# Kernel optimization log

Measured on AMD Instinct MI355X. Metric: run time of the kernel, lower is better.

Reference implementation:

```python
import jax, jax.numpy as jnp
import numpy as np

T_ITERS, N_SLOTS, INPUT_DIM, DIM = 6, 256, 1024, 1024
MLP_DIM = DIM // 2
B, C, H, W = 8, 1024, 64, 64
LN_EPS = 1e-5


def _ln(x, g, b):
    m = jnp.mean(x, axis=-1, keepdims=True)
    v = jnp.mean(jnp.square(x - m), axis=-1, keepdims=True)
    return (x - m) * jax.lax.rsqrt(v + LN_EPS) * g + b


def setup_inputs() -> dict:
    key = jax.random.key(0)
    ks = jax.random.split(key, 8)
    x = jax.random.normal(ks[0], (B, C, H, W), dtype=jnp.float32)
    templates_init = jax.random.normal(ks[1], (1, N_SLOTS, DIM), dtype=jnp.float32)
    # torch Linear weight is [out,in]; store as [in,out] for x @ W
    s_in = 1.0 / np.sqrt(INPUT_DIM)
    s_d = 1.0 / np.sqrt(DIM)
    Wq = jax.random.uniform(ks[2], (DIM, DIM), jnp.float32, -s_d, s_d)
    Wk = jax.random.uniform(ks[3], (INPUT_DIM, DIM), jnp.float32, -s_in, s_in)
    Wv = jax.random.uniform(ks[4], (INPUT_DIM, DIM), jnp.float32, -s_in, s_in)
    W1 = jax.random.uniform(ks[5], (DIM, MLP_DIM), jnp.float32, -s_d, s_d)
    b1 = jnp.zeros((MLP_DIM,), jnp.float32)
    s_m = 1.0 / np.sqrt(MLP_DIM)
    W2 = jax.random.uniform(ks[6], (MLP_DIM, DIM), jnp.float32, -s_m, s_m)
    b2 = jnp.zeros((DIM,), jnp.float32)
    return {
        "x": x, "templates_init": templates_init,
        "Wq": Wq, "Wk": Wk, "Wv": Wv,
        "ln_in_g": jnp.ones((INPUT_DIM,), jnp.float32), "ln_in_b": jnp.zeros((INPUT_DIM,), jnp.float32),
        "ln_t_g": jnp.ones((DIM,), jnp.float32), "ln_t_b": jnp.zeros((DIM,), jnp.float32),
        "ln_m_g": jnp.ones((DIM,), jnp.float32), "ln_m_b": jnp.zeros((DIM,), jnp.float32),
        "W1": W1, "b1": b1, "W2": W2, "b2": b2,
    }


def reference(x, templates_init, Wq, Wk, Wv, ln_in_g, ln_in_b, ln_t_g, ln_t_b,
              ln_m_g, ln_m_b, W1, b1, W2, b2):
    Bv, Cv, Hv, Wd = x.shape
    scale = DIM ** (-0.5)
    xr = x.reshape(Bv, Cv, Hv * Wd).transpose(0, 2, 1)  # [B, L, C]
    xn = _ln(xr, ln_in_g, ln_in_b)
    k = xn @ Wk  # [B, L, D]
    v = xn @ Wv  # [B, L, D]
    templates = jnp.broadcast_to(templates_init, (Bv, N_SLOTS, DIM))
    attn = None
    for _ in range(T_ITERS):
        t_prev = templates
        t = _ln(t_prev, ln_t_g, ln_t_b)
        q = (t @ Wq) * scale  # [B, N, D]
        logits = jnp.einsum('bnd,bld->bln', q, k)
        attn = jax.nn.softmax(logits, axis=-1) + 1e-8  # softmax over N
        attn = attn / jnp.sum(attn, axis=-2, keepdims=True)  # renorm over L
        templates = t_prev + jnp.einsum('bld,bln->bnd', v, attn)
        m = _ln(templates, ln_m_g, ln_m_b)
        templates = templates + jax.nn.relu(m @ W1 + b1) @ W2 + b2
    out_templates = templates.transpose(0, 2, 1)[:, :, :, None]  # [B, D, N, 1]
    out_attn = attn.transpose(0, 2, 1).reshape(Bv, N_SLOTS, Hv, Wd)
    return (out_templates, out_attn)
```

## Files before the change

kernel.cpp:

```cpp
#include <hip/hip_runtime.h>

#define EPS_ 1e-5f
#define SCALE_ 0.03125f

typedef __attribute__((ext_vector_type(8))) short short8;
typedef __attribute__((ext_vector_type(4))) float f32x4;
typedef unsigned short u16;

__device__ __forceinline__ float bf2f(u16 s) {
  return __uint_as_float(((unsigned int)s) << 16);
}
__device__ __forceinline__ u16 f2bf(float f) {
  unsigned int u = __float_as_uint(f);
  unsigned int r = 0x7FFFu + ((u >> 16) & 1u);
  return (u16)((u + r) >> 16);
}

__device__ __forceinline__ void gload16(const void* g, void* l) {
  __builtin_amdgcn_global_load_lds(
      (const __attribute__((address_space(1))) unsigned int*)g,
      (__attribute__((address_space(3))) unsigned int*)l, 16, 0, 0);
}

__global__ __launch_bounds__(256) void ln_part(const float* __restrict__ x,
                                               float* __restrict__ ps,
                                               float* __restrict__ ps2) {
  int tl = threadIdx.x & 63;
  int cg = threadIdx.x >> 6;
  int lblk = blockIdx.x >> 3;
  int cchunk = blockIdx.x & 7;
  int row = lblk * 64 + tl;
  int bb = row >> 12, l = row & 4095;
  const float* xp = x + (long)bb * 4194304L + l;
  int c0 = cchunk * 128 + cg;
  float s = 0.f, s2 = 0.f;
#pragma unroll
  for (int i = 0; i < 32; ++i) {
    float v = xp[(long)(c0 + i * 4) * 4096];
    s += v; s2 += v * v;
  }
  __shared__ float sh[2][4][64];
  sh[0][cg][tl] = s; sh[1][cg][tl] = s2;
  __syncthreads();
  if (threadIdx.x < 64) {
    float ts = sh[0][0][tl] + sh[0][1][tl] + sh[0][2][tl] + sh[0][3][tl];
    float t2 = sh[1][0][tl] + sh[1][1][tl] + sh[1][2][tl] + sh[1][3][tl];
    ps[cchunk * 32768 + row] = ts;
    ps2[cchunk * 32768 + row] = t2;
  }
}

__global__ __launch_bounds__(256) void ln_red(const float* __restrict__ ps,
                                              const float* __restrict__ ps2,
                                              float* __restrict__ meanp,
                                              float* __restrict__ rstdp) {
  int row = blockIdx.x * 256 + threadIdx.x;
  float s = 0.f, s2 = 0.f;
#pragma unroll
  for (int k = 0; k < 8; ++k) {
    s += ps[k * 32768 + row];
    s2 += ps2[k * 32768 + row];
  }
  float mu = s * (1.0f / 1024.0f);
  float var = s2 * (1.0f / 1024.0f) - mu * mu;
  meanp[row] = mu;
  rstdp[row] = rsqrtf(var + EPS_);
}

__global__ __launch_bounds__(256) void xn_make(const float* __restrict__ x,
                                               u16* __restrict__ xn,
                                               const float* __restrict__ meanp,
                                               const float* __restrict__ rstdp,
                                               const float* __restrict__ g,
                                               const float* __restrict__ beta) {
  __shared__ float tile[32][33];
  int b = blockIdx.z;
  int ct = blockIdx.y * 32;
  int lt = blockIdx.x * 32;
  int tx = threadIdx.x & 31, ty = threadIdx.x >> 5;
  const float* xp = x + (long)b * 4194304;
  int l = lt + tx;
  float mu = meanp[(b << 12) + l];
  float rs = rstdp[(b << 12) + l];
#pragma unroll
  for (int k = 0; k < 32; k += 8) {
    int c = ct + ty + k;
    float v = xp[(long)c * 4096 + l];
    tile[ty + k][tx] = (v - mu) * rs * g[c] + beta[c];
  }
  __syncthreads();
  u16* xq = xn + (long)b * 4194304;
#pragma unroll
  for (int k = 0; k < 32; k += 8) {
    int ll = lt + ty + k;
    xq[(long)ll * 1024 + ct + tx] = f2bf(tile[tx][ty + k]);
  }
}

__global__ __launch_bounds__(256) void transpose_f32(const float* __restrict__ src,
                                                     float* __restrict__ dst,
                                                     int R, int Cc, long sSrc, long sDst) {
  __shared__ float tile[32][33];
  int z = blockIdx.z;
  int rt = blockIdx.y * 32, ct = blockIdx.x * 32;
  int tx = threadIdx.x & 31, ty = threadIdx.x >> 5;
  const float* s = src + (long)z * sSrc;
  float* d = dst + (long)z * sDst;
#pragma unroll
  for (int k = 0; k < 32; k += 8) tile[ty + k][tx] = s[(long)(rt + ty + k) * Cc + ct + tx];
  __syncthreads();
#pragma unroll
  for (int k = 0; k < 32; k += 8) d[(long)(ct + ty + k) * R + rt + tx] = tile[tx][ty + k];
}

__global__ __launch_bounds__(256) void tcast(const float* __restrict__ src,
                                             u16* __restrict__ dst, int R, int C) {
  __shared__ float tile[32][33];
  int rt = blockIdx.y * 32, ct = blockIdx.x * 32;
  int tx = threadIdx.x & 31, ty = threadIdx.x >> 5;
#pragma unroll
  for (int k = 0; k < 32; k += 8) tile[ty + k][tx] = src[(long)(rt + ty + k) * C + ct + tx];
  __syncthreads();
#pragma unroll
  for (int k = 0; k < 32; k += 8) dst[(long)(ct + ty + k) * R + rt + tx] = f2bf(tile[tx][ty + k]);
}

__global__ __launch_bounds__(256) void castbf(const float* __restrict__ in,
                                              u16* __restrict__ out) {
  long i = (long)blockIdx.x * 256 + threadIdx.x;
  out[i] = f2bf(in[i]);
}

enum { E_BF16 = 0, E_SCALEBF = 1, E_F32 = 2, E_UPD = 3, E_RELU = 4, E_ADDB = 5 };

template <int EPI, int KSPLIT = 1>
__global__ __launch_bounds__(256) void mgemm(
    const u16* __restrict__ A, const u16* __restrict__ Bt, void* __restrict__ Cv,
    int K, int lda, int ldb, int ldc, long sA, long sB, long sC,
    const float* __restrict__ bias, const float* __restrict__ colsum) {
  __shared__ u16 Als[128 * 64];
  __shared__ u16 Bls[128 * 64];
  const int tid = threadIdx.x;
  const int zb = (KSPLIT == 1) ? blockIdx.z : blockIdx.z / KSPLIT;
  const int ks = (KSPLIT == 1) ? 0 : blockIdx.z % KSPLIT;
  const int bm = blockIdx.y * 128;
  const int bn = blockIdx.x * 128;
  A += (long)zb * sA;
  Bt += (long)zb * sB;
  const int kpart = K / KSPLIT;
  const int kbase = ks * kpart;
  const int lane = tid & 63;
  const int w = tid >> 6;
  const int wm = (w & 1) * 64, wn = (w >> 1) * 64;
  const int fr = lane & 15;
  const int fq = lane >> 4;
  f32x4 acc[4][4] = {};

  const int srow = tid >> 3;
  const int sko = (tid & 7) << 3;
  const u16* Ag = A + (long)(bm + srow) * lda + kbase + sko;
  const u16* Bg = Bt + (long)(bn + srow) * ldb + kbase + sko;
  u16* Al = Als + tid * 8;
  u16* Bl = Bls + tid * 8;
  const long astep = 32L * lda;
  const long bstep = 32L * ldb;

  for (int k0 = 0; k0 < kpart; k0 += 64) {
#pragma unroll
    for (int i = 0; i < 4; ++i) {
      gload16(Ag + i * astep + k0, Al + i * 2048);
      gload16(Bg + i * bstep + k0, Bl + i * 2048);
    }
    __syncthreads();
#pragma unroll
    for (int kc = 0; kc < 2; ++kc) {
      const int koff = kc * 32 + fq * 8;
      short8 af[4], bf[4];
#pragma unroll
      for (int i = 0; i < 4; ++i)
        af[i] = *(const short8*)&Als[(wm + i * 16 + fr) * 64 + koff];
#pragma unroll
      for (int j = 0; j < 4; ++j)
        bf[j] = *(const short8*)&Bls[(wn + j * 16 + fr) * 64 + koff];
#pragma unroll
      for (int i = 0; i < 4; ++i)
#pragma unroll
        for (int j = 0; j < 4; ++j)
          acc[i][j] = __builtin_amdgcn_mfma_f32_16x16x32_bf16(af[i], bf[j], acc[i][j], 0, 0, 0);
    }
    __syncthreads();
  }

#pragma unroll
  for (int i = 0; i < 4; ++i) {
#pragma unroll
    for (int j = 0; j < 4; ++j) {
      int gc = bn + wn + j * 16 + fr;
#pragma unroll
      for (int r = 0; r < 4; ++r) {
        int gr = bm + wm + i * 16 + fq * 4 + r;
        float v = acc[i][j][r];
        if constexpr (EPI == E_BF16) {
          ((u16*)Cv + (long)zb * sC)[(long)gr * ldc + gc] = f2bf(v);
        } else if constexpr (EPI == E_SCALEBF) {
          ((u16*)Cv + (long)zb * sC)[(long)gr * ldc + gc] = f2bf(v * SCALE_);
        } else if constexpr (EPI == E_F32) {
          ((float*)Cv + (long)zb * sC)[(long)gr * ldc + gc] = v;
        } else if constexpr (EPI == E_UPD) {
          float* C = (float*)Cv + (long)zb * sC;
          float add = v * (1.0f / colsum[zb * 256 + gr]);
          if constexpr (KSPLIT > 1) atomicAdd(&C[(long)gr * ldc + gc], add);
          else C[(long)gr * ldc + gc] += add;
        } else if constexpr (EPI == E_RELU) {
          float h = v + bias[gc];
          ((u16*)Cv + (long)zb * sC)[(long)gr * ldc + gc] = f2bf(h > 0.f ? h : 0.f);
        } else {
          float* C = (float*)Cv + (long)zb * sC;
          C[(long)gr * ldc + gc] += v + bias[gc];
        }
      }
    }
  }
}

__global__ __launch_bounds__(256) void row_ln_bf(const float* __restrict__ in,
                                                 u16* __restrict__ out,
                                                 const float* __restrict__ g,
                                                 const float* __restrict__ bvec) {
  long base = (long)blockIdx.x * 1024;
  int c = threadIdx.x << 2;
  float4 xv = *(const float4*)&in[base + c];
  float s = xv.x + xv.y + xv.z + xv.w;
  float s2 = xv.x * xv.x + xv.y * xv.y + xv.z * xv.z + xv.w * xv.w;
#pragma unroll
  for (int off = 32; off > 0; off >>= 1) {
    s += __shfl_down(s, off);
    s2 += __shfl_down(s2, off);
  }
  __shared__ float sh[8];
  if ((threadIdx.x & 63) == 0) {
    sh[threadIdx.x >> 6] = s;
    sh[4 + (threadIdx.x >> 6)] = s2;
  }
  __syncthreads();
  float ts = sh[0] + sh[1] + sh[2] + sh[3];
  float t2 = sh[4] + sh[5] + sh[6] + sh[7];
  float mu = ts * (1.0f / 1024.0f);
  float rs = rsqrtf(t2 * (1.0f / 1024.0f) - mu * mu + EPS_);
  ushort4 o;
  o.x = f2bf((xv.x - mu) * rs * g[c + 0] + bvec[c + 0]);
  o.y = f2bf((xv.y - mu) * rs * g[c + 1] + bvec[c + 1]);
  o.z = f2bf((xv.z - mu) * rs * g[c + 2] + bvec[c + 2]);
  o.w = f2bf((xv.w - mu) * rs * g[c + 3] + bvec[c + 3]);
  *(ushort4*)&out[base + c] = o;
}

__global__ __launch_bounds__(256) void softmax_tile(const float* __restrict__ lg,
                                                    u16* __restrict__ attnbf) {
  __shared__ float tile[256 * 36];
  __shared__ float pmax[8][32], psum[8][32];
  __shared__ float fm[32], fi[32];
  const int z = blockIdx.y;
  const int lt = blockIdx.x * 32;
  const int t = threadIdx.x;
  const float* base = lg + (long)z * 1048576 + lt;
  const int lr = t >> 3, lcg = (t & 7) << 2;
#pragma unroll
  for (int p = 0; p < 8; ++p) {
    int n = p * 32 + lr;
    float4 v = *(const float4*)&base[(long)n * 4096 + lcg];
    *(float4*)&tile[n * 36 + lcg] = v;
  }
  __syncthreads();
  const int l = t & 31, g = t >> 5;
  float m = -1e30f;
#pragma unroll
  for (int i = 0; i < 32; ++i) m = fmaxf(m, tile[(g * 32 + i) * 36 + l]);
  pmax[g][l] = m;
  __syncthreads();
  if (t < 32) {
    float mm = pmax[0][t];
#pragma unroll
    for (int k = 1; k < 8; ++k) mm = fmaxf(mm, pmax[k][t]);
    fm[t] = mm;
  }
  __syncthreads();
  float mx = fm[l];
  float s = 0.f;
#pragma unroll
  for (int i = 0; i < 32; ++i) {
    int n = g * 32 + i;
    float e = __expf(tile[n * 36 + l] - mx);
    tile[n * 36 + l] = e;
    s += e;
  }
  psum[g][l] = s;
  __syncthreads();
  if (t < 32) {
    float ss = psum[0][t];
#pragma unroll
    for (int k = 1; k < 8; ++k) ss += psum[k][t];
    fi[t] = 1.0f / ss;
  }
  __syncthreads();
  float inv = fi[l];
  u16* outp = attnbf + (long)z * 1048576 + lt + l;
#pragma unroll
  for (int i = 0; i < 32; ++i) {
    int n = g * 32 + i;
    outp[(long)n * 4096] = f2bf(tile[n * 36 + l] * inv + 1e-8f);
  }
}

__global__ __launch_bounds__(256) void row_sum_bf(const u16* __restrict__ a,
                                                  float* __restrict__ colsum) {
  long base = (long)blockIdx.x * 4096 + threadIdx.x * 16;
  float s = 0.f;
#pragma unroll
  for (int i = 0; i < 16; i += 4) {
    ushort4 v = *(const ushort4*)&a[base + i];
    s += bf2f(v.x) + bf2f(v.y) + bf2f(v.z) + bf2f(v.w);
  }
#pragma unroll
  for (int off = 32; off > 0; off >>= 1) s += __shfl_down(s, off);
  __shared__ float sh[4];
  if ((threadIdx.x & 63) == 0) sh[threadIdx.x >> 6] = s;
  __syncthreads();
  if (threadIdx.x == 0) colsum[blockIdx.x] = sh[0] + sh[1] + sh[2] + sh[3];
}

__global__ __launch_bounds__(256) void bcast_tmpl(const float* __restrict__ tinit,
                                                  float* __restrict__ tmpl) {
  long i = (long)blockIdx.x * 256 + threadIdx.x;
  tmpl[i] = tinit[i & 262143];
}

__global__ __launch_bounds__(256) void attn_final_g(const u16* __restrict__ ab,
                                                    const float* __restrict__ cs,
                                                    float* __restrict__ out) {
  long i = (long)blockIdx.x * 256 + threadIdx.x;
  out[i] = bf2f(ab[i]) / cs[i >> 12];
}

extern "C" void kernel_launch(void* const* d_in, const int* in_sizes, int n_in,
                              void* d_out, int out_size, void* d_ws, size_t ws_size,
                              hipStream_t stream) {
  const float* x       = (const float*)d_in[0];
  const float* tinit   = (const float*)d_in[1];
  const float* Wq      = (const float*)d_in[2];
  const float* Wk      = (const float*)d_in[3];
  const float* Wv      = (const float*)d_in[4];
  const float* ln_in_g = (const float*)d_in[5];
  const float* ln_in_b = (const float*)d_in[6];
  const float* ln_t_g  = (const float*)d_in[7];
  const float* ln_t_b  = (const float*)d_in[8];
  const float* ln_m_g  = (const float*)d_in[9];
  const float* ln_m_b  = (const float*)d_in[10];
  const float* W1      = (const float*)d_in[11];
  const float* b1      = (const float*)d_in[12];
  const float* W2      = (const float*)d_in[13];
  const float* b2      = (const float*)d_in[14];
  (void)in_sizes; (void)n_in; (void)out_size; (void)ws_size;

  char* ws = (char*)d_ws;
  size_t off = 0;
  auto alloc = [&](size_t bytes) {
    void* p = ws + off;
    off += (bytes + 255) & ~(size_t)255;
    return p;
  };
  float* meanp   = (float*)alloc(32768ULL * 4);
  float* rstdp   = (float*)alloc(32768ULL * 4);
  float* ps      = (float*)alloc(262144ULL * 4);
  float* ps2     = (float*)alloc(262144ULL * 4);
  u16* xn        = (u16*)alloc(33554432ULL * 2);
  u16* vT        = (u16*)alloc(33554432ULL * 2);
  u16* attnbf    = (u16*)alloc(8388608ULL * 2);
  u16* tln       = (u16*)alloc(2097152ULL * 2);
  u16* qk        = (u16*)alloc(2097152ULL * 2);
  u16* hidden    = (u16*)alloc(1048576ULL * 2);
  float* tmpl    = (float*)alloc(2097152ULL * 4);
  u16* WqkT      = (u16*)alloc(1048576ULL * 2);
  u16* WvT       = (u16*)alloc(1048576ULL * 2);
  u16* W1T       = (u16*)alloc(524288ULL * 2);
  u16* W2T       = (u16*)alloc(524288ULL * 2);
  float* colsum  = (float*)alloc(2048ULL * 4);

  u16* Wkbf = attnbf;
  u16* Wqbf = attnbf + 1048576;

  float* outT        = (float*)d_out;
  float* attnOutBase = (float*)d_out + 2097152;
  float* logitsS     = attnOutBase;

  dim3 blk(256);

  ln_part<<<dim3(4096), blk, 0, stream>>>(x, ps, ps2);
  ln_red<<<dim3(128), blk, 0, stream>>>(ps, ps2, meanp, rstdp);

  castbf<<<dim3(4096), blk, 0, stream>>>(Wk, Wkbf);
  castbf<<<dim3(4096), blk, 0, stream>>>(Wq, Wqbf);
  mgemm<E_SCALEBF><<<dim3(8, 8, 1), blk, 0, stream>>>(
      Wkbf, Wqbf, WqkT, 1024, 1024, 1024, 1024, 0, 0, 0, nullptr, nullptr);
  tcast<<<dim3(32, 32), blk, 0, stream>>>(Wv, WvT, 1024, 1024);
  tcast<<<dim3(16, 32), blk, 0, stream>>>(W1, W1T, 1024, 512);
  tcast<<<dim3(32, 16), blk, 0, stream>>>(W2, W2T, 512, 1024);

  xn_make<<<dim3(128, 32, 8), blk, 0, stream>>>(x, xn, meanp, rstdp, ln_in_g, ln_in_b);
  mgemm<E_BF16><<<dim3(32, 8, 8), blk, 0, stream>>>(
      WvT, xn, vT, 1024, 1024, 1024, 4096, 0, 4194304L, 4194304L, nullptr, nullptr);
  bcast_tmpl<<<dim3(8192), blk, 0, stream>>>(tinit, tmpl);

  for (int it = 0; it < 6; ++it) {
    row_ln_bf<<<dim3(2048), blk, 0, stream>>>(tmpl, tln, ln_t_g, ln_t_b);
    mgemm<E_BF16><<<dim3(8, 16, 1), blk, 0, stream>>>(
        tln, WqkT, qk, 1024, 1024, 1024, 1024, 0, 0, 0, nullptr, nullptr);
    mgemm<E_F32><<<dim3(32, 2, 8), blk, 0, stream>>>(
        qk, xn, logitsS, 1024, 1024, 1024, 4096, 262144L, 4194304L, 1048576L,
        nullptr, nullptr);
    softmax_tile<<<dim3(128, 8), blk, 0, stream>>>(logitsS, attnbf);
    row_sum_bf<<<dim3(2048), blk, 0, stream>>>(attnbf, colsum);
    mgemm<E_UPD, 2><<<dim3(8, 2, 16), blk, 0, stream>>>(
        attnbf, vT, tmpl, 4096, 4096, 4096, 1024, 1048576L, 4194304L, 262144L,
        nullptr, colsum);
    row_ln_bf<<<dim3(2048), blk, 0, stream>>>(tmpl, tln, ln_m_g, ln_m_b);
    mgemm<E_RELU><<<dim3(4, 16, 1), blk, 0, stream>>>(
        tln, W1T, hidden, 1024, 1024, 1024, 512, 0, 0, 0, b1, nullptr);
    mgemm<E_ADDB><<<dim3(8, 16, 1), blk, 0, stream>>>(
        hidden, W2T, tmpl, 512, 512, 512, 1024, 0, 0, 0, b2, nullptr);
  }

  attn_final_g<<<dim3(32768), blk, 0, stream>>>(attnbf, colsum, attnOutBase);
  transpose_f32<<<dim3(32, 8, 8), blk, 0, stream>>>(
      tmpl, outT, 256, 1024, 262144L, 262144L);
}
```

Measured before the change: 1.477 ms.

## Fuse logits GEMM, softmax over slots, and column sums into one kernel

Replaces the fp32 logits GEMM, the separate softmax kernel and the row-sum kernel with a single kernel. Each block computes all 256 slots for a 64-column L tile, so the softmax over slots can be done in registers. It writes bf16 attention directly and accumulates the per-slot sums with atomics, while the LN kernel zeroes colsum. This removes the fp32 logits round trip through global memory and two launches per iteration. In exchange it launches only 512 blocks, uses an unpipelined K loop with a large accumulator tile, and adds atomics.

```diff
diff --git a/kernel.cpp b/kernel.cpp
--- a/kernel.cpp
+++ b/kernel.cpp
@@ -223,10 +223,138 @@
   }
 }
 
+__global__ __launch_bounds__(256) void fls(const u16* __restrict__ qk,
+                                           const u16* __restrict__ xn,
+                                           u16* __restrict__ attnbf,
+                                           float* __restrict__ colsum) {
+  __shared__ u16 Als[256 * 64];
+  __shared__ u16 Bls[64 * 64];
+  __shared__ float sred[4][64];
+  __shared__ float ssum[4][64];
+  const int tid = threadIdx.x;
+  const int z = blockIdx.z;
+  const int l0 = blockIdx.x * 64;
+  const u16* A = qk + (long)z * 262144;
+  const u16* B = xn + (long)z * 4194304;
+  const int lane = tid & 63;
+  const int w = tid >> 6;
+  const int wm = w * 64;
+  const int fr = lane & 15, fq = lane >> 4;
+  f32x4 acc[4][4] = {};
+
+  const int srow = tid >> 3;
+  const int sko = (tid & 7) << 3;
+  const u16* Ag = A + (long)srow * 1024 + sko;
+  const u16* Bg = B + (long)(l0 + srow) * 1024 + sko;
+  u16* Al = Als + tid * 8;
+  u16* Bl = Bls + tid * 8;
+
+  for (int k0 = 0; k0 < 1024; k0 += 64) {
+#pragma unroll
+    for (int i = 0; i < 8; ++i)
+      gload16(Ag + (long)i * 32768 + k0, Al + i * 2048);
+#pragma unroll
+    for (int i = 0; i < 2; ++i)
+      gload16(Bg + (long)i * 32768 + k0, Bl + i * 2048);
+    __syncthreads();
+#pragma unroll
+    for (int kc = 0; kc < 2; ++kc) {
+      const int koff = kc * 32 + fq * 8;
+      short8 af[4], bf[4];
+#pragma unroll
+      for (int i = 0; i < 4; ++i)
+        af[i] = *(const short8*)&Als[(wm + i * 16 + fr) * 64 + koff];
+#pragma unroll
+      for (int j = 0; j < 4; ++j)
+        bf[j] = *(const short8*)&Bls[(j * 16 + fr) * 64 + koff];
+#pragma unroll
+      for (int i = 0; i < 4; ++i)
+#pragma unroll
+        for (int j = 0; j < 4; ++j)
+          acc[i][j] = __builtin_amdgcn_mfma_f32_16x16x32_bf16(af[i], bf[j], acc[i][j], 0, 0, 0);
+    }
+    __syncthreads();
+  }
+
+  float mj[4];
+#pragma unroll
+  for (int j = 0; j < 4; ++j) {
+    float m = acc[0][j][0];
+#pragma unroll
+    for (int i = 0; i < 4; ++i)
+#pragma unroll
+      for (int r = 0; r < 4; ++r) m = fmaxf(m, acc[i][j][r]);
+    m = fmaxf(m, __shfl_xor(m, 16));
+    m = fmaxf(m, __shfl_xor(m, 32));
+    mj[j] = m;
+  }
+  if (fq == 0) {
+#pragma unroll
+    for (int j = 0; j < 4; ++j) sred[w][j * 16 + fr] = mj[j];
+  }
+  __syncthreads();
+  float M4[4];
+#pragma unroll
+  for (int j = 0; j < 4; ++j) {
+    int c = j * 16 + fr;
+    M4[j] = fmaxf(fmaxf(sred[0][c], sred[1][c]), fmaxf(sred[2][c], sred[3][c]));
+  }
+  float pj[4] = {0.f, 0.f, 0.f, 0.f};
+#pragma unroll
+  for (int i = 0; i < 4; ++i)
+#pragma unroll
+    for (int j = 0; j < 4; ++j)
+#pragma unroll
+      for (int r = 0; r < 4; ++r) {
+        float e = __expf(acc[i][j][r] - M4[j]);
+        acc[i][j][r] = e;
+        pj[j] += e;
+      }
+#pragma unroll
+  for (int j = 0; j < 4; ++j) {
+    pj[j] += __shfl_xor(pj[j], 16);
+    pj[j] += __shfl_xor(pj[j], 32);
+  }
+  if (fq == 0) {
+#pragma unroll
+    for (int j = 0; j < 4; ++j) ssum[w][j * 16 + fr] = pj[j];
+  }
+  __syncthreads();
+  float inv[4];
+#pragma unroll
+  for (int j = 0; j < 4; ++j) {
+    int c = j * 16 + fr;
+    inv[j] = 1.0f / (ssum[0][c] + ssum[1][c] + ssum[2][c] + ssum[3][c]);
+  }
+  u16* outp = attnbf + (long)z * 1048576;
+#pragma unroll
+  for (int i = 0; i < 4; ++i) {
+#pragma unroll
+    for (int r = 0; r < 4; ++r) {
+      int n = wm + i * 16 + fq * 4 + r;
+      float cs = 0.f;
+#pragma unroll
+      for (int j = 0; j < 4; ++j) {
+        float a = acc[i][j][r] * inv[j] + 1e-8f;
+        u16 ab = f2bf(a);
+        outp[(long)n * 4096 + l0 + j * 16 + fr] = ab;
+        cs += bf2f(ab);
+      }
+      cs += __shfl_xor(cs, 1);
+      cs += __shfl_xor(cs, 2);
+      cs += __shfl_xor(cs, 4);
+      cs += __shfl_xor(cs, 8);
+      if (fr == 0) atomicAdd(&colsum[z * 256 + n], cs);
+    }
+  }
+}
+
 __global__ __launch_bounds__(256) void row_ln_bf(const float* __restrict__ in,
                                                  u16* __restrict__ out,
                                                  const float* __restrict__ g,
-                                                 const float* __restrict__ bvec) {
+                                                 const float* __restrict__ bvec,
+                                                 float* __restrict__ cz) {
+  if (cz && blockIdx.x < 8) cz[blockIdx.x * 256 + threadIdx.x] = 0.f;
   long base = (long)blockIdx.x * 1024;
   int c = threadIdx.x << 2;
   float4 xv = *(const float4*)&in[base + c];
@@ -253,80 +381,6 @@
   o.z = f2bf((xv.z - mu) * rs * g[c + 2] + bvec[c + 2]);
   o.w = f2bf((xv.w - mu) * rs * g[c + 3] + bvec[c + 3]);
   *(ushort4*)&out[base + c] = o;
-}
-
-__global__ __launch_bounds__(256) void softmax_tile(const float* __restrict__ lg,
-                                                    u16* __restrict__ attnbf) {
-  __shared__ float tile[256 * 36];
-  __shared__ float pmax[8][32], psum[8][32];
-  __shared__ float fm[32], fi[32];
-  const int z = blockIdx.y;
-  const int lt = blockIdx.x * 32;
-  const int t = threadIdx.x;
-  const float* base = lg + (long)z * 1048576 + lt;
-  const int lr = t >> 3, lcg = (t & 7) << 2;
-#pragma unroll
-  for (int p = 0; p < 8; ++p) {
-    int n = p * 32 + lr;
-    float4 v = *(const float4*)&base[(long)n * 4096 + lcg];
-    *(float4*)&tile[n * 36 + lcg] = v;
-  }
-  __syncthreads();
-  const int l = t & 31, g = t >> 5;
-  float m = -1e30f;
-#pragma unroll
-  for (int i = 0; i < 32; ++i) m = fmaxf(m, tile[(g * 32 + i) * 36 + l]);
-  pmax[g][l] = m;
-  __syncthreads();
-  if (t < 32) {
-    float mm = pmax[0][t];
-#pragma unroll
-    for (int k = 1; k < 8; ++k) mm = fmaxf(mm, pmax[k][t]);
-    fm[t] = mm;
-  }
-  __syncthreads();
-  float mx = fm[l];
-  float s = 0.f;
-#pragma unroll
-  for (int i = 0; i < 32; ++i) {
-    int n = g * 32 + i;
-    float e = __expf(tile[n * 36 + l] - mx);
-    tile[n * 36 + l] = e;
-    s += e;
-  }
-  psum[g][l] = s;
-  __syncthreads();
-  if (t < 32) {
-    float ss = psum[0][t];
-#pragma unroll
-    for (int k = 1; k < 8; ++k) ss += psum[k][t];
-    fi[t] = 1.0f / ss;
-  }
-  __syncthreads();
-  float inv = fi[l];
-  u16* outp = attnbf + (long)z * 1048576 + lt + l;
-#pragma unroll
-  for (int i = 0; i < 32; ++i) {
-    int n = g * 32 + i;
-    outp[(long)n * 4096] = f2bf(tile[n * 36 + l] * inv + 1e-8f);
-  }
-}
-
-__global__ __launch_bounds__(256) void row_sum_bf(const u16* __restrict__ a,
-                                                  float* __restrict__ colsum) {
-  long base = (long)blockIdx.x * 4096 + threadIdx.x * 16;
-  float s = 0.f;
-#pragma unroll
-  for (int i = 0; i < 16; i += 4) {
-    ushort4 v = *(const ushort4*)&a[base + i];
-    s += bf2f(v.x) + bf2f(v.y) + bf2f(v.z) + bf2f(v.w);
-  }
-#pragma unroll
-  for (int off = 32; off > 0; off >>= 1) s += __shfl_down(s, off);
-  __shared__ float sh[4];
-  if ((threadIdx.x & 63) == 0) sh[threadIdx.x >> 6] = s;
-  __syncthreads();
-  if (threadIdx.x == 0) colsum[blockIdx.x] = sh[0] + sh[1] + sh[2] + sh[3];
 }
 
 __global__ __launch_bounds__(256) void bcast_tmpl(const float* __restrict__ tinit,
@@ -391,7 +445,6 @@
 
   float* outT        = (float*)d_out;
   float* attnOutBase = (float*)d_out + 2097152;
-  float* logitsS     = attnOutBase;
 
   dim3 blk(256);
 
@@ -412,18 +465,14 @@
   bcast_tmpl<<<dim3(8192), blk, 0, stream>>>(tinit, tmpl);
 
   for (int it = 0; it < 6; ++it) {
-    row_ln_bf<<<dim3(2048), blk, 0, stream>>>(tmpl, tln, ln_t_g, ln_t_b);
+    row_ln_bf<<<dim3(2048), blk, 0, stream>>>(tmpl, tln, ln_t_g, ln_t_b, colsum);
     mgemm<E_BF16><<<dim3(8, 16, 1), blk, 0, stream>>>(
         tln, WqkT, qk, 1024, 1024, 1024, 1024, 0, 0, 0, nullptr, nullptr);
-    mgemm<E_F32><<<dim3(32, 2, 8), blk, 0, stream>>>(
-        qk, xn, logitsS, 1024, 1024, 1024, 4096, 262144L, 4194304L, 1048576L,
-        nullptr, nullptr);
-    softmax_tile<<<dim3(128, 8), blk, 0, stream>>>(logitsS, attnbf);
-    row_sum_bf<<<dim3(2048), blk, 0, stream>>>(attnbf, colsum);
+    fls<<<dim3(64, 1, 8), blk, 0, stream>>>(qk, xn, attnbf, colsum);
     mgemm<E_UPD, 2><<<dim3(8, 2, 16), blk, 0, stream>>>(
         attnbf, vT, tmpl, 4096, 4096, 4096, 1024, 1048576L, 4194304L, 262144L,
         nullptr, colsum);
-    row_ln_bf<<<dim3(2048), blk, 0, stream>>>(tmpl, tln, ln_m_g, ln_m_b);
+    row_ln_bf<<<dim3(2048), blk, 0, stream>>>(tmpl, tln, ln_m_g, ln_m_b, nullptr);
     mgemm<E_RELU><<<dim3(4, 16, 1), blk, 0, stream>>>(
         tln, W1T, hidden, 1024, 1024, 1024, 512, 0, 0, 0, b1, nullptr);
     mgemm<E_ADDB><<<dim3(8, 16, 1), blk, 0, stream>>>(
```

After: 1.439 ms. 1.03x faster.
